# Kernel tuning notes

Hardware: AMD Instinct MI355X
Metric: run time of the kernel (lower is better)

The kernel has to match this reference:

```python
import jax, jax.numpy as jnp
import numpy as np

BLANK = 1
NEG = -1e30


def ctc_loss_mean(logprobs, targets, input_lengths, target_lengths):
    """CTC loss, log-space forward DP, matching torch.nn.CTCLoss(blank=1, reduction='mean').
    logprobs: [B,T,V] log-softmaxed; targets: [B,L] int; lengths: [B] int."""
    B, T, V = logprobs.shape
    L = targets.shape[1]
    S = 2 * L + 1  # extended label seq: blank interleaved
    ext = jnp.full((B, S), BLANK, dtype=targets.dtype)
    ext = ext.at[:, 1::2].set(targets)
    # lp_ext[b,t,s] = logprobs[b,t,ext[b,s]]
    lp_ext = jnp.take_along_axis(logprobs, jnp.broadcast_to(ext[:, None, :], (B, T, S)), axis=2)
    ext_m2 = jnp.pad(ext, ((0, 0), (2, 0)), constant_values=BLANK)[:, :S]
    skip_ok = (ext != BLANK) & (ext != ext_m2)  # [B,S] allow s-2 transition

    alpha = jnp.full((B, S), NEG, dtype=logprobs.dtype)
    alpha = alpha.at[:, 0].set(lp_ext[:, 0, 0])
    alpha = alpha.at[:, 1].set(jnp.where(target_lengths > 0, lp_ext[:, 0, 1], NEG))

    def step(alpha, inp):
        lp_t, t = inp  # lp_t: [B,S]
        a1 = jnp.pad(alpha, ((0, 0), (1, 0)), constant_values=NEG)[:, :S]
        a2 = jnp.pad(alpha, ((0, 0), (2, 0)), constant_values=NEG)[:, :S]
        a2 = jnp.where(skip_ok, a2, NEG)
        new = jnp.logaddexp(jnp.logaddexp(alpha, a1), a2) + lp_t
        alpha = jnp.where((t < input_lengths)[:, None], new, alpha)
        return alpha, None

    lp_tbs = jnp.transpose(lp_ext, (1, 0, 2))  # [T,B,S]
    alpha, _ = jax.lax.scan(step, alpha, (lp_tbs[1:], jnp.arange(1, T)))

    idx_last = 2 * target_lengths  # final blank position
    idx_prev = jnp.maximum(idx_last - 1, 0)
    a_last = jnp.take_along_axis(alpha, idx_last[:, None], axis=1)[:, 0]
    a_prev = jnp.where(target_lengths > 0,
                       jnp.take_along_axis(alpha, idx_prev[:, None], axis=1)[:, 0], NEG)
    per_sample = -jnp.logaddexp(a_last, a_prev)
    tl = jnp.maximum(target_lengths, 1).astype(logprobs.dtype)
    return jnp.mean(per_sample / tl)  # torch 'mean': divide by target_len, then batch mean


def setup_inputs() -> dict:
    key = jax.random.key(0)
    ks = jax.random.split(key, 8)
    B, Ssrc, D, STRIDE, V, L = 32, 512, 512, 4, 512, 256
    representation = jax.random.normal(ks[0], (B, Ssrc, D), dtype=jnp.float32)
    encoder_mask = jnp.ones((B, Ssrc), dtype=bool)
    targets = jax.random.randint(ks[1], (B, L), 2, V)  # avoid blank=1 and 0
    target_mask = jnp.ones((B, L), dtype=bool)
    def lin(k, fin, fout):
        return jax.random.normal(k, (fin, fout), dtype=jnp.float32) / np.sqrt(fin)
    return {
        "representation": representation,
        "encoder_mask": encoder_mask,
        "targets": targets,
        "target_mask": target_mask,
        "W_exp": lin(ks[2], D, STRIDE * D),
        "b_exp": jnp.zeros((STRIDE * D,), jnp.float32),
        "W1": lin(ks[3], D, 2 * D),
        "b1": jnp.zeros((2 * D,), jnp.float32),
        "W2": lin(ks[4], 2 * D, V),
        "b2": jnp.zeros((V,), jnp.float32),
    }


def reference(representation, encoder_mask, targets, target_mask,
              W_exp, b_exp, W1, b1, W2, b2):
    B = representation.shape[0]
    dim = W_exp.shape[0]
    seq_lengths = encoder_mask.astype(jnp.int32).sum(1)
    stride = W_exp.shape[1] // dim
    # expand: Linear(dim, stride*dim) then fold stride into time axis
    states = (jnp.einsum("bsd,de->bse", representation, W_exp) + b_exp).reshape(B, -1, dim)
    h = jax.nn.relu(jnp.einsum("btd,dh->bth", states, W1) + b1)
    logits = jnp.einsum("bth,hv->btv", h, W2) + b2  # dropout: eval-mode identity
    logprobs = jax.nn.log_softmax(logits, axis=-1)
    target_lengths = target_mask.astype(jnp.int32).sum(1)
    out_lengths = stride * seq_lengths
    loss = ctc_loss_mean(logprobs, targets, out_lengths, target_lengths)
    loss = jnp.where(jnp.isnan(loss) | jnp.isinf(loss), jnp.zeros_like(loss), loss)
    return logprobs, out_lengths, loss
```

## Files before the change

kernel.cpp:

```cpp
#include <hip/hip_runtime.h>
#include <math.h>

#define B_ 32
#define SSRC 512
#define D_ 512
#define STRIDE_ 4
#define V_ 512
#define L_ 256
#define T_ (SSRC * STRIDE_)
#define S_ (2 * L_ + 1)
#define BLANKI 1
#define PSTRIDE 264
#define BOOST 4096.0f
#define BOOST_BITS 12

typedef __attribute__((ext_vector_type(8))) short bf16x8;
typedef __attribute__((ext_vector_type(4))) float f32x4;

__device__ __forceinline__ unsigned short bf16r(float x) {
    unsigned u = __float_as_uint(x);
    return (unsigned short)((u + 0x7fffu + ((u >> 16) & 1u)) >> 16);
}
__device__ __forceinline__ float bf2f(unsigned short u) {
    return __uint_as_float((unsigned)u << 16);
}
__device__ __forceinline__ void gl_lds16(const unsigned short* g, unsigned short* l) {
    __builtin_amdgcn_global_load_lds(
        (const __attribute__((address_space(1))) unsigned int*)g,
        (__attribute__((address_space(3))) unsigned int*)l, 16, 0, 0);
}

__global__ __launch_bounds__(256) void combine_bias(
    const float* __restrict__ b_exp, const float* __restrict__ W1,
    const float* __restrict__ b1, float* __restrict__ bc)
{
    int j = blockIdx.x * 256 + threadIdx.x;
    int k = j >> 10, h = j & 1023;
    float s = b1[h];
    const float* be = b_exp + k * 512;
    for (int d = 0; d < 512; ++d)
        s = fmaf(be[d], W1[d * 1024 + h], s);
    bc[j] = s;
}

__global__ __launch_bounds__(256) void transpose_cvt(
    const float* __restrict__ in, unsigned short* __restrict__ out, int R, int C)
{
// ... 70 lines not shown
        for (int mi = 0; mi < 4; ++mi)
            af[mi] = *(const bf16x8*)&As[cur][wm + mi * 16 + (lane & 15)][(lane >> 4) * 8];
#pragma unroll
        for (int ni = 0; ni < 4; ++ni)
            bfr[ni] = *(const bf16x8*)&Bs[cur][wn + ni * 16 + (lane & 15)][(lane >> 4) * 8];
#pragma unroll
        for (int mi = 0; mi < 4; ++mi)
#pragma unroll
            for (int ni = 0; ni < 4; ++ni)
                acc[mi][ni] = __builtin_amdgcn_mfma_f32_16x16x32_bf16(
                    af[mi], bfr[ni], acc[mi][ni], 0, 0, 0);
    }

#pragma unroll
    for (int ni = 0; ni < 4; ++ni) {
        int gcol = bn + wn + ni * 16 + (lane & 15);
        float bv = BIAS ? bias[gcol] : 0.f;
#pragma unroll
        for (int mi = 0; mi < 4; ++mi) {
#pragma unroll
            for (int q2 = 0; q2 < 4; ++q2) {
                int grow = bm + wm + mi * 16 + ((lane >> 4) << 2) + q2;
                float x = acc[mi][ni][q2] + bv;
                if (RELU) x = fmaxf(x, 0.f);
                if (OUTBF16)
                    Cb[(size_t)grow * ldc + gcol] = bf16r(x);
                else
                    Cf[(size_t)grow * ldc + gcol] = x;
            }
        }
    }
}

__global__ __launch_bounds__(1024) void gemm2_lsm(
    const unsigned short* __restrict__ H,
    const unsigned short* __restrict__ W2T,
    const float* __restrict__ b2,
    const int* __restrict__ targets,
    float* __restrict__ lp,
    unsigned short* __restrict__ P)
{
    __shared__ __align__(16) char SMEM[81920];
    unsigned short* As = (unsigned short*)SMEM;
    unsigned short* Bs = (unsigned short*)(SMEM + 16384);
    float* redm = (float*)SMEM;
    float* reds = (float*)(SMEM + 4096);
    unsigned short* prt = (unsigned short*)(SMEM + 8192);
    int* s_tg = (int*)(SMEM + 8192 + 65536);

    const int tid = threadIdx.x;
    const int wid = tid >> 6, lane = tid & 63;
    const int wr = wid >> 3, wc = wid & 7;
    const int r0 = blockIdx.x * 128;
    const int b = r0 >> 11;

    auto stage = [&](int buf, int k0) {
#pragma unroll
        for (int ii = 0; ii < 3; ++ii) {
            int issue = wid + 16 * ii;
            if (issue < 8) {
                int rr = issue * 16;
                gl_lds16(H + (size_t)(r0 + rr + (lane >> 2)) * 1024 + k0 + (lane & 3) * 8,
                         &As[buf * 4096 + rr * 32]);
            } else if (issue < 40) {
                int rr = (issue - 8) * 16;
                gl_lds16(W2T + (size_t)(rr + (lane >> 2)) * 1024 + k0 + (lane & 3) * 8,
                         &Bs[buf * 16384 + rr * 32]);
            }
        }
    };

    f32x4 acc[4][4] = {};
    stage(0, 0);
    for (int t = 0; t < 32; ++t) {
        const int cur = t & 1;
        __syncthreads();
        if (t + 1 < 32) stage(cur ^ 1, (t + 1) * 32);
        bf16x8 af[4], bfr[4];
#pragma unroll
        for (int mi = 0; mi < 4; ++mi)
            af[mi] = *(const bf16x8*)&As[cur * 4096 +
                        (wr * 64 + mi * 16 + (lane & 15)) * 32 + (lane >> 4) * 8];
#pragma unroll
        for (int ni = 0; ni < 4; ++ni)
            bfr[ni] = *(const bf16x8*)&Bs[cur * 16384 +
                        (wc * 64 + ni * 16 + (lane & 15)) * 32 + (lane >> 4) * 8];
#pragma unroll
// ... 77 lines not shown
            for (int g = 1; g < 8; ++g) st += reds[g * 128 + row];
            rm[mi][q] = rm[mi][q] + logf(st);
        }

#pragma unroll
    for (int p = 0; p < 2; ++p) {
        if (wr == p) {
#pragma unroll
            for (int mi = 0; mi < 4; ++mi)
#pragma unroll
                for (int q = 0; q < 4; ++q) {
                    int rloc = mi * 16 + ((lane >> 4) << 2) + q;
                    int row = wr * 64 + rloc;
#pragma unroll
                    for (int ni = 0; ni < 4; ++ni) {
                        int col = wc * 64 + ni * 16 + (lane & 15);
                        float lpv = acc[mi][ni][q] - rm[mi][q];
                        lp[(size_t)(r0 + row) * 512 + col] = lpv;
                        prt[rloc * 512 + col] = bf16r(expf(lpv) * BOOST);
                    }
                }
        }
        __syncthreads();
        if (tid < 514) {
            int j = tid % 257;
            int rh = tid / 257;
            int col = (j < 256) ? s_tg[j] : BLANKI;
#pragma unroll 4
            for (int r = rh * 32; r < rh * 32 + 32; ++r)
                P[(size_t)(r0 + p * 64 + r) * PSTRIDE + j] = prt[r * 512 + col];
        }
        __syncthreads();
    }
}

struct Pr5 { float pb, p1, p3, p5, p7; };

__device__ __forceinline__ Pr5 ldrowf(const unsigned short* rp, int l)
{
    ushort4 q = *(const ushort4*)(rp + 4 * l);
    Pr5 r;
    r.pb = bf2f(rp[256]);
    r.p1 = bf2f(q.x); r.p3 = bf2f(q.y); r.p5 = bf2f(q.z); r.p7 = bf2f(q.w);
    return r;
}

#define REP16(OP) OP(0) OP(1) OP(2) OP(3) OP(4) OP(5) OP(6) OP(7) \
                  OP(8) OP(9) OP(10) OP(11) OP(12) OP(13) OP(14) OP(15)

__global__ __launch_bounds__(512) void ctc_fwd_bwd(
    const unsigned short* __restrict__ P,
    const int* __restrict__ enc_mask, const int* __restrict__ targets,
    const int* __restrict__ tgt_mask,
    float* __restrict__ out_len_f,
    double* __restrict__ AV, double* __restrict__ BV,
    int* __restrict__ EF, int* __restrict__ EB,
    int* __restrict__ ILv, int* __restrict__ tl_out)
{
    const int wid = threadIdx.x >> 6;
    const int l = threadIdx.x & 63;
    const int task = blockIdx.x * 8 + wid;
    const int b = task & 31;
    const bool isf = task < 32;

    int se = 0, st = 0;
    {
        const int* em = enc_mask + (size_t)b * SSRC;
#pragma unroll
        for (int i = 0; i < 8; ++i) se += (em[i * 64 + l] != 0) ? 1 : 0;
        const int* tm = tgt_mask + (size_t)b * L_;
#pragma unroll
        for (int i = 0; i < 4; ++i) st += (tm[i * 64 + l] != 0) ? 1 : 0;
#pragma unroll
        for (int off = 32; off; off >>= 1) {
            se += __shfl_xor(se, off);
            st += __shfl_xor(st, off);
        }
    }
    const int tl = st;
    const int IL = STRIDE_ * se;
    const int h = (IL > 0) ? ((IL - 1) >> 1) : 0;

    const int4 tg = ((const int4*)(targets + (size_t)b * L_))[l];
    int prevw = __shfl_up(tg.w, 1);
    if (l == 0) prevw = BLANKI;
    const bool k1 = (tg.x != BLANKI) && (tg.x != prevw);
    const bool k3 = (tg.y != BLANKI) && (tg.y != tg.x);
    const bool k5 = (tg.z != BLANKI) && (tg.z != tg.y);
    const bool k7 = (tg.w != BLANKI) && (tg.w != tg.z);

    const unsigned short* Pb = P + (size_t)b * T_ * PSTRIDE;

    double a0 = 0, a1 = 0, a2 = 0, a3 = 0, a4 = 0, a5 = 0, a6 = 0, a7 = 0, a8 = 0;
    int Ei = 0;

    auto rescale9 = [&]() {
        double m = fmax(fmax(fmax(a0, a1), fmax(a2, a3)),
                        fmax(fmax(a4, a5), fmax(fmax(a6, a7), a8)));
        int e = (int)((__double_as_longlong(m) >> 52) & 0x7ff);
#pragma unroll
        for (int off = 1; off < 64; off <<= 1) {
            int o = __shfl_xor(e, off);
            e = o > e ? o : e;
        }
        int sh = 1023 - e;
        double sc = __longlong_as_double(((long long)(sh + 1023)) << 52);
        Ei += e - 1023;
        a0 *= sc; a1 *= sc; a2 *= sc; a3 *= sc; a4 *= sc;
        a5 *= sc; a6 *= sc; a7 *= sc; a8 *= sc;
    };

    if (isf) {
        if (l == 0) {
            a0 = (double)bf2f(Pb[256]);
            if (tl > 0) a1 = (double)bf2f(Pb[0]);
        }
        auto fstep = [&](const Pr5& r) {
            double pb = (double)r.pb, p1 = (double)r.p1, p3 = (double)r.p3;
            double p5 = (double)r.p5, p7 = (double)r.p7;
            double u1 = __shfl_up(a7, 1);
            if (l == 0) u1 = 0.0;
            double n0 = (a0 + u1) * pb;
            double n1 = (a0 + a1 + (k1 ? u1 : 0.0)) * p1;
            double n2 = (a1 + a2) * pb;
            double n3 = (a2 + a3 + (k3 ? a1 : 0.0)) * p3;
            double n4 = (a3 + a4) * pb;
            double n5 = (a4 + a5 + (k5 ? a3 : 0.0)) * p5;
            double n6 = (a5 + a6) * pb;
            double n7 = (a6 + a7 + (k7 ? a5 : 0.0)) * p7;
            double n8 = (l == 63) ? (a7 + a8) * pb : 0.0;
            a0 = n0; a1 = n1; a2 = n2; a3 = n3; a4 = n4;
            a5 = n5; a6 = n6; a7 = n7; a8 = n8;
        };
        const int nst = h;
        if (nst > 0) {
            Pr5 q0, q1, q2, q3, q4, q5, q6, q7, q8, q9, q10, q11, q12, q13, q14, q15;
#define LDI(i) { int ti = 1 + i; if (ti > nst) ti = nst; \
                 q##i = ldrowf(Pb + (size_t)ti * PSTRIDE, l); }
            REP16(LDI)
#undef LDI
            int t = 1;
            while (t + 15 <= nst) {
#define STP(i) { fstep(q##i); int ti = t + 16 + i; if (ti > nst) ti = nst; \
                 q##i = ldrowf(Pb + (size_t)ti * PSTRIDE, l); }
                REP16(STP)
#undef STP
                rescale9();
                t += 16;
            }
            int rem = nst - t + 1;
#define TLS(i) if (i < rem) fstep(q##i);
            REP16(TLS)
#undef TLS
        }
        rescale9();
        double* av = AV + b * 520;
        av[l * 8 + 0] = a0; av[l * 8 + 1] = a1; av[l * 8 + 2] = a2; av[l * 8 + 3] = a3;
        av[l * 8 + 4] = a4; av[l * 8 + 5] = a5; av[l * 8 + 6] = a6; av[l * 8 + 7] = a7;
        if (l == 63) av[512] = a8;
        if (l == 0) {
            EF[b] = Ei; ILv[b] = IL; tl_out[b] = tl;
            out_len_f[b] = (float)IL;
        }
    } else {
        {
            int s0 = l * 8;
            int e0 = 2 * tl, e1 = 2 * tl - 1;
            a0 = (s0 + 0 == e0 || (tl > 0 && s0 + 0 == e1)) ? 1.0 : 0.0;
            a1 = (s0 + 1 == e0 || (tl > 0 && s0 + 1 == e1)) ? 1.0 : 0.0;
            a2 = (s0 + 2 == e0 || (tl > 0 && s0 + 2 == e1)) ? 1.0 : 0.0;
            a3 = (s0 + 3 == e0 || (tl > 0 && s0 + 3 == e1)) ? 1.0 : 0.0;
            a4 = (s0 + 4 == e0 || (tl > 0 && s0 + 4 == e1)) ? 1.0 : 0.0;
            a5 = (s0 + 5 == e0 || (tl > 0 && s0 + 5 == e1)) ? 1.0 : 0.0;
            a6 = (s0 + 6 == e0 || (tl > 0 && s0 + 6 == e1)) ? 1.0 : 0.0;
            a7 = (s0 + 7 == e0 || (tl > 0 && s0 + 7 == e1)) ? 1.0 : 0.0;
            if (l == 63) a8 = (512 == e0) ? 1.0 : 0.0;
        }
        float knff = __shfl_down(k1 ? 1.f : 0.f, 1);
        if (l == 63) knff = 0.f;
        const double knf = (double)knff;
        auto bstep = [&](const Pr5& r) {
            double pb = (double)r.pb, p1 = (double)r.p1, p3 = (double)r.p3;
            double p5 = (double)r.p5, p7 = (double)r.p7;
            double g0 = a0 * pb, g1 = a1 * p1, g2 = a2 * pb, g3 = a3 * p3;
            double g4 = a4 * pb, g5 = a5 * p5, g6 = a6 * pb, g7 = a7 * p7;
            double g8 = (l == 63) ? a8 * pb : 0.0;
            double d1 = __shfl_down(g0, 1);
            double d2 = __shfl_down(g1, 1);
            if (l == 63) { d1 = g8; d2 = 0.0; }
            double m0 = g0 + g1;
            double m1 = g1 + g2 + (k3 ? g3 : 0.0);
            double m2 = g2 + g3;
            double m3 = g3 + g4 + (k5 ? g5 : 0.0);
            double m4 = g4 + g5;
            double m5 = g5 + g6 + (k7 ? g7 : 0.0);
            double m6 = g6 + g7;
            double m7 = g7 + d1 + knf * d2;
            double m8 = (l == 63) ? g8 : 0.0;
            a0 = m0; a1 = m1; a2 = m2; a3 = m3; a4 = m4;
            a5 = m5; a6 = m6; a7 = m7; a8 = m8;
        };
        const int nbs = IL - 1 - h;
        if (nbs > 0) {
            const int rmin = h + 1;
            Pr5 q0, q1, q2, q3, q4, q5, q6, q7, q8, q9, q10, q11, q12, q13, q14, q15;
#define LDB(i) { int ri = IL - 1 - i; if (ri < rmin) ri = rmin; \
                 q##i = ldrowf(Pb + (size_t)ri * PSTRIDE, l); }
            REP16(LDB)
#undef LDB
            int j = 0;
            while (j + 16 <= nbs) {
#define STB(i) { bstep(q##i); int ri = IL - 1 - (j + 16 + i); if (ri < rmin) ri = rmin; \
                 q##i = ldrowf(Pb + (size_t)ri * PSTRIDE, l); }
                REP16(STB)
#undef STB
                rescale9();
                j += 16;
            }
            int rem = nbs - j;
#define TLB(i) if (i < rem) bstep(q##i);
            REP16(TLB)
#undef TLB
        }
        rescale9();
        double* bv = BV + b * 520;
        bv[l * 8 + 0] = a0; bv[l * 8 + 1] = a1; bv[l * 8 + 2] = a2; bv[l * 8 + 3] = a3;
        bv[l * 8 + 4] = a4; bv[l * 8 + 5] = a5; bv[l * 8 + 6] = a6; bv[l * 8 + 7] = a7;
        if (l == 63) bv[512] = a8;
        if (l == 0) EB[b] = Ei;
    }
}

__global__ __launch_bounds__(64) void ctc_combine(
    const double* __restrict__ AV, const double* __restrict__ BV,
    const int* __restrict__ EF, const int* __restrict__ EB,
    const int* __restrict__ ILv, float* __restrict__ per_sample)
{
    const int b = blockIdx.x, l = threadIdx.x;
    const double* av = AV + b * 520;
    const double* bv = BV + b * 520;
    double s = 0.0;
#pragma unroll
    for (int i = 0; i < 8; ++i)
        s += av[l * 8 + i] * bv[l * 8 + i];
    if (l == 63) s += av[512] * bv[512];
#pragma unroll
    for (int off = 1; off < 64; off <<= 1) s += __shfl_xor(s, off);
    if (l == 0) {
        double lg = log(s) +
            (double)(EF[b] + EB[b] - BOOST_BITS * ILv[b]) * 0.6931471805599453;
        per_sample[b] = -(float)lg;
    }
}

__global__ __launch_bounds__(64) void ctc_loss_final(
    const float* __restrict__ per_sample, const int* __restrict__ tl,
    float* __restrict__ out_loss)
{
    int tid = threadIdx.x;
    float v = 0.f;
    if (tid < B_) {
        int t = tl[tid] < 1 ? 1 : tl[tid];
        v = per_sample[tid] / (float)t;
// ... 10 lines not shown
extern "C" void kernel_launch(void* const* d_in, const int* in_sizes, int n_in,
                              void* d_out, int out_size, void* d_ws, size_t ws_size,
                              hipStream_t stream)
{
    (void)in_sizes; (void)n_in; (void)out_size; (void)ws_size;

    const float* rep      = (const float*)d_in[0];
    const int*   enc_mask = (const int*)d_in[1];
    const int*   targets  = (const int*)d_in[2];
    const int*   tgt_mask = (const int*)d_in[3];
    const float* W_exp    = (const float*)d_in[4];
    const float* b_exp    = (const float*)d_in[5];
    const float* W1       = (const float*)d_in[6];
    const float* b1       = (const float*)d_in[7];
    const float* W2       = (const float*)d_in[8];
    const float* b2       = (const float*)d_in[9];

    float* out       = (float*)d_out;
    float* logprobs  = out;
    float* out_len_f = out + (size_t)B_ * T_ * V_;
    float* out_loss  = out_len_f + B_;
    unsigned short* Hd = (unsigned short*)d_out;

    unsigned short* WcT = (unsigned short*)d_ws;
    float* bc           = (float*)(WcT + (size_t)4096 * 512);
    float* per_sample   = bc + 4096;
    int*   tl_out       = (int*)(per_sample + 64);
    unsigned short* P   = (unsigned short*)(tl_out + 64);
    double* AV          = (double*)(P + (size_t)65536 * PSTRIDE);
    double* BV          = AV + 32 * 520;
    int*   EF           = (int*)(BV + 32 * 520);
    int*   EB           = EF + 32;
    int*   ILv          = EB + 32;
    unsigned short* repb   = P;
    unsigned short* W_expb = P + (size_t)16384 * 512;
    unsigned short* W1T    = W_expb + (size_t)512 * 2048;
    unsigned short* W2T    = WcT;

    cvt_f32_bf16<<<8192, 256, 0, stream>>>(rep, repb, (16384 * 512) / 4);
    cvt_f32_bf16<<<1024, 256, 0, stream>>>(W_exp, W_expb, (512 * 2048) / 4);
    transpose_cvt<<<dim3(32, 16), dim3(32, 8), 0, stream>>>(W1, W1T, 512, 1024);

    gemm_mfma<false, true, false><<<dim3(4, 8, 4), 256, 0, stream>>>(
        W1T, 512, 0, W_expb, 2048, 512, WcT, 512, (long)1024 * 512, nullptr, 512);
    combine_bias<<<16, 256, 0, stream>>>(b_exp, W1, b1, bc);

    gemm_mfma<true, true, true><<<dim3(32, 128), 256, 0, stream>>>(
        repb, 512, 0, WcT, 512, 0, Hd, 4096, 0, bc, 512);

    transpose_cvt<<<dim3(16, 32), dim3(32, 8), 0, stream>>>(W2, W2T, 1024, 512);

    gemm2_lsm<<<512, 1024, 0, stream>>>(Hd, W2T, b2, targets, logprobs, P);

    ctc_fwd_bwd<<<8, 512, 0, stream>>>(P, enc_mask, targets, tgt_mask,
                                       out_len_f, AV, BV, EF, EB, ILv, tl_out);
    ctc_combine<<<32, 64, 0, stream>>>(AV, BV, EF, EB, ILv, per_sample);
    ctc_loss_final<<<1, 64, 0, stream>>>(per_sample, tl_out, out_loss);
}
```

Measured before the change: 488.1 us.

## Fuse CTC forward/backward into GEMM2 kernel with per-chunk readiness flags

Merges the CTC forward/backward recursion into the GEMM2+log-softmax kernel. The first 64 blocks act as single-wave consumers that spin on per-sample, per-128-row chunk flags. Producer blocks publish each chunk with a release atomic after a threadfence. Producer chunk order is interleaved from both ends, so the forward and backward consumers can start early. This overlaps the serial CTC recursion with the GEMM and removes one kernel launch. It relies on consumer blocks being scheduled alongside producers without deadlock, and each consumer block reserves a 1024-thread slot plus 80KB of LDS while only one wave does work.

```diff
diff --git a/kernel.cpp b/kernel.cpp
--- a/kernel.cpp
+++ b/kernel.cpp
@@ -13,6 +13,7 @@
 #define PSTRIDE 264
 #define BOOST 4096.0f
 #define BOOST_BITS 12
+#define NCONS 64
 
 typedef __attribute__((ext_vector_type(8))) short bf16x8;
 typedef __attribute__((ext_vector_type(4))) float f32x4;
@@ -149,15 +150,234 @@
     }
 }
 
-__global__ __launch_bounds__(1024) void gemm2_lsm(
+struct Pr5 { float pb, p1, p3, p5, p7; };
+
+__device__ __forceinline__ Pr5 ldrowf(const unsigned short* rp, int l)
+{
+    ushort4 q = *(const ushort4*)(rp + 4 * l);
+    Pr5 r;
+    r.pb = bf2f(rp[256]);
+    r.p1 = bf2f(q.x); r.p3 = bf2f(q.y); r.p5 = bf2f(q.z); r.p7 = bf2f(q.w);
+    return r;
+}
+
+#define REP16(OP) OP(0) OP(1) OP(2) OP(3) OP(4) OP(5) OP(6) OP(7) \
+                  OP(8) OP(9) OP(10) OP(11) OP(12) OP(13) OP(14) OP(15)
+
+__global__ __launch_bounds__(1024) void gemm2_lsm_ctc(
     const unsigned short* __restrict__ H,
     const unsigned short* __restrict__ W2T,
     const float* __restrict__ b2,
     const int* __restrict__ targets,
+    const int* __restrict__ enc_mask, const int* __restrict__ tgt_mask,
     float* __restrict__ lp,
-    unsigned short* __restrict__ P)
+    unsigned short* __restrict__ P,
+    int* __restrict__ flags,
+    float* __restrict__ out_len_f,
+    double* __restrict__ AV, double* __restrict__ BV,
+    int* __restrict__ EF, int* __restrict__ EB,
+    int* __restrict__ ILv, int* __restrict__ tl_out)
 {
     __shared__ __align__(16) char SMEM[81920];
+    const int tid = threadIdx.x;
+
+    if (blockIdx.x < NCONS) {
+        if (tid >= 64) return;
+        const int task = blockIdx.x;
+        const int b = task & 31;
+        const bool isf = task < 32;
+        const int l = tid;
+
+        int se = 0, st = 0;
+        {
+            const int* em = enc_mask + (size_t)b * SSRC;
+#pragma unroll
+            for (int i = 0; i < 8; ++i) se += (em[i * 64 + l] != 0) ? 1 : 0;
+            const int* tm = tgt_mask + (size_t)b * L_;
+#pragma unroll
+            for (int i = 0; i < 4; ++i) st += (tm[i * 64 + l] != 0) ? 1 : 0;
+#pragma unroll
+            for (int off = 32; off; off >>= 1) {
+                se += __shfl_xor(se, off);
+                st += __shfl_xor(st, off);
+            }
+        }
+        const int tl = st;
+        const int IL = STRIDE_ * se;
+        const int h = (IL > 0) ? ((IL - 1) >> 1) : 0;
+
+        const int4 tg = ((const int4*)(targets + (size_t)b * L_))[l];
+        int prevw = __shfl_up(tg.w, 1);
+        if (l == 0) prevw = BLANKI;
+        const bool k1 = (tg.x != BLANKI) && (tg.x != prevw);
+        const bool k3 = (tg.y != BLANKI) && (tg.y != tg.x);
+        const bool k5 = (tg.z != BLANKI) && (tg.z != tg.y);
+        const bool k7 = (tg.w != BLANKI) && (tg.w != tg.z);
+
+        const unsigned short* Pb = P + (size_t)b * T_ * PSTRIDE;
+
+        double a0 = 0, a1 = 0, a2 = 0, a3 = 0, a4 = 0, a5 = 0, a6 = 0, a7 = 0, a8 = 0;
+        int Ei = 0;
+
+        auto rescale9 = [&]() {
+            double m = fmax(fmax(fmax(a0, a1), fmax(a2, a3)),
+                            fmax(fmax(a4, a5), fmax(fmax(a6, a7), a8)));
+            int e = (int)((__double_as_longlong(m) >> 52) & 0x7ff);
+#pragma unroll
+            for (int off = 1; off < 64; off <<= 1) {
+                int o = __shfl_xor(e, off);
+                e = o > e ? o : e;
+            }
+            int sh = 1023 - e;
+            double sc = __longlong_as_double(((long long)(sh + 1023)) << 52);
+            Ei += e - 1023;
+            a0 *= sc; a1 *= sc; a2 *= sc; a3 *= sc; a4 *= sc;
+            a5 *= sc; a6 *= sc; a7 *= sc; a8 *= sc;
+        };
+        auto waitflag = [&](int c) {
+            const int f = b * 16 + c;
+            while (__hip_atomic_load(&flags[f], __ATOMIC_ACQUIRE,
+                                     __HIP_MEMORY_SCOPE_AGENT) == 0)
+                __builtin_amdgcn_s_sleep(16);
+        };
+
+        if (isf) {
+            int nw = 0;
+            auto waitup = [&](int row) {
+                int tc = row >> 7; if (tc > 15) tc = 15;
+                while (nw <= tc) { waitflag(nw); ++nw; }
+            };
+            waitup(0);
+            if (l == 0) {
+                a0 = (double)bf2f(Pb[256]);
+                if (tl > 0) a1 = (double)bf2f(Pb[0]);
+            }
+            auto fstep = [&](const Pr5& r) {
+                double pb = (double)r.pb, p1 = (double)r.p1, p3 = (double)r.p3;
+                double p5 = (double)r.p5, p7 = (double)r.p7;
+                double u1 = __shfl_up(a7, 1);
+                if (l == 0) u1 = 0.0;
+                double n0 = (a0 + u1) * pb;
+                double n1 = (a0 + a1 + (k1 ? u1 : 0.0)) * p1;
+                double n2 = (a1 + a2) * pb;
+                double n3 = (a2 + a3 + (k3 ? a1 : 0.0)) * p3;
+                double n4 = (a3 + a4) * pb;
+                double n5 = (a4 + a5 + (k5 ? a3 : 0.0)) * p5;
+                double n6 = (a5 + a6) * pb;
+                double n7 = (a6 + a7 + (k7 ? a5 : 0.0)) * p7;
+                double n8 = (l == 63) ? (a7 + a8) * pb : 0.0;
+                a0 = n0; a1 = n1; a2 = n2; a3 = n3; a4 = n4;
+                a5 = n5; a6 = n6; a7 = n7; a8 = n8;
+            };
+            const int nst = h;
+            if (nst > 0) {
+                waitup(nst < 47 ? nst : 47);
+                Pr5 q0, q1, q2, q3, q4, q5, q6, q7, q8, q9, q10, q11, q12, q13, q14, q15;
+#define LDI(i) { int ti = 1 + i; if (ti > nst) ti = nst; \
+                 q##i = ldrowf(Pb + (size_t)ti * PSTRIDE, l); }
+                REP16(LDI)
+#undef LDI
+                int t = 1;
+                while (t + 15 <= nst) {
+                    { int r2 = t + 47; if (r2 > nst) r2 = nst; waitup(r2); }
+#define STP(i) { fstep(q##i); int ti = t + 16 + i; if (ti > nst) ti = nst; \
+                 q##i = ldrowf(Pb + (size_t)ti * PSTRIDE, l); }
+                    REP16(STP)
+#undef STP
+                    rescale9();
+                    t += 16;
+                }
+                int rem = nst - t + 1;
+#define TLS(i) if (i < rem) fstep(q##i);
+                REP16(TLS)
+#undef TLS
+            }
+            rescale9();
+            double* av = AV + b * 520;
+            av[l * 8 + 0] = a0; av[l * 8 + 1] = a1; av[l * 8 + 2] = a2; av[l * 8 + 3] = a3;
+            av[l * 8 + 4] = a4; av[l * 8 + 5] = a5; av[l * 8 + 6] = a6; av[l * 8 + 7] = a7;
+            if (l == 63) av[512] = a8;
+            if (l == 0) {
+                EF[b] = Ei; ILv[b] = IL; tl_out[b] = tl;
+                out_len_f[b] = (float)IL;
+            }
+        } else {
+            int nb = 15;
+            auto waitdn = [&](int row) {
+                int tc = row >> 7; if (tc < 0) tc = 0;
+                while (nb >= tc) { waitflag(nb); --nb; }
+            };
+            {
+                int s0 = l * 8;
+                int e0 = 2 * tl, e1 = 2 * tl - 1;
+                a0 = (s0 + 0 == e0 || (tl > 0 && s0 + 0 == e1)) ? 1.0 : 0.0;
+                a1 = (s0 + 1 == e0 || (tl > 0 && s0 + 1 == e1)) ? 1.0 : 0.0;
+                a2 = (s0 + 2 == e0 || (tl > 0 && s0 + 2 == e1)) ? 1.0 : 0.0;
+                a3 = (s0 + 3 == e0 || (tl > 0 && s0 + 3 == e1)) ? 1.0 : 0.0;
+                a4 = (s0 + 4 == e0 || (tl > 0 && s0 + 4 == e1)) ? 1.0 : 0.0;
+                a5 = (s0 + 5 == e0 || (tl > 0 && s0 + 5 == e1)) ? 1.0 : 0.0;
+                a6 = (s0 + 6 == e0 || (tl > 0 && s0 + 6 == e1)) ? 1.0 : 0.0;
+                a7 = (s0 + 7 == e0 || (tl > 0 && s0 + 7 == e1)) ? 1.0 : 0.0;
+                if (l == 63) a8 = (512 == e0) ? 1.0 : 0.0;
+            }
+            float knff = __shfl_down(k1 ? 1.f : 0.f, 1);
+            if (l == 63) knff = 0.f;
+            const double knf = (double)knff;
+            auto bstep = [&](const Pr5& r) {
+                double pb = (double)r.pb, p1 = (double)r.p1, p3 = (double)r.p3;
+                double p5 = (double)r.p5, p7 = (double)r.p7;
+                double g0 = a0 * pb, g1 = a1 * p1, g2 = a2 * pb, g3 = a3 * p3;
+                double g4 = a4 * pb, g5 = a5 * p5, g6 = a6 * pb, g7 = a7 * p7;
+                double g8 = (l == 63) ? a8 * pb : 0.0;
+                double d1 = __shfl_down(g0, 1);
+                double d2 = __shfl_down(g1, 1);
+                if (l == 63) { d1 = g8; d2 = 0.0; }
+                double m0 = g0 + g1;
+                double m1 = g1 + g2 + (k3 ? g3 : 0.0);
+                double m2 = g2 + g3;
+                double m3 = g3 + g4 + (k5 ? g5 : 0.0);
+                double m4 = g4 + g5;
+                double m5 = g5 + g6 + (k7 ? g7 : 0.0);
+                double m6 = g6 + g7;
+                double m7 = g7 + d1 + knf * d2;
+                double m8 = (l == 63) ? g8 : 0.0;
+                a0 = m0; a1 = m1; a2 = m2; a3 = m3; a4 = m4;
+                a5 = m5; a6 = m6; a7 = m7; a8 = m8;
+            };
+            const int nbs = IL - 1 - h;
+            if (nbs > 0) {
+                const int rmin = h + 1;
+                { int r2 = IL - 1 - 47; if (r2 < rmin) r2 = rmin; waitdn(r2); }
+                Pr5 q0, q1, q2, q3, q4, q5, q6, q7, q8, q9, q10, q11, q12, q13, q14, q15;
+#define LDB(i) { int ri = IL - 1 - i; if (ri < rmin) ri = rmin; \
+                 q##i = ldrowf(Pb + (size_t)ri * PSTRIDE, l); }
+                REP16(LDB)
+#undef LDB
+                int j = 0;
+                while (j + 16 <= nbs) {
+                    { int r2 = IL - 1 - (j + 47); if (r2 < rmin) r2 = rmin; waitdn(r2); }
+#define STB(i) { bstep(q##i); int ri = IL - 1 - (j + 16 + i); if (ri < rmin) ri = rmin; \
+                 q##i = ldrowf(Pb + (size_t)ri * PSTRIDE, l); }
+                    REP16(STB)
+#undef STB
+                    rescale9();
+                    j += 16;
+                }
+                int rem = nbs - j;
+#define TLB(i) if (i < rem) bstep(q##i);
+                REP16(TLB)
+#undef TLB
+            }
+            rescale9();
+            double* bv = BV + b * 520;
+            bv[l * 8 + 0] = a0; bv[l * 8 + 1] = a1; bv[l * 8 + 2] = a2; bv[l * 8 + 3] = a3;
+            bv[l * 8 + 4] = a4; bv[l * 8 + 5] = a5; bv[l * 8 + 6] = a6; bv[l * 8 + 7] = a7;
+            if (l == 63) bv[512] = a8;
+            if (l == 0) EB[b] = Ei;
+        }
+        return;
+    }
+
     unsigned short* As = (unsigned short*)SMEM;
     unsigned short* Bs = (unsigned short*)(SMEM + 16384);
     float* redm = (float*)SMEM;
@@ -165,11 +385,15 @@
     unsigned short* prt = (unsigned short*)(SMEM + 8192);
     int* s_tg = (int*)(SMEM + 8192 + 65536);
 
-    const int tid = threadIdx.x;
+    const int pid = blockIdx.x - NCONS;
+    const int smp = pid & 31;
+    const int pc = pid >> 5;
+    const int chk = (pc & 1) ? (15 - (pc >> 1)) : (pc >> 1);
+    const int r0 = smp * 2048 + chk * 128;
+    const int b = smp;
+
     const int wid = tid >> 6, lane = tid & 63;
     const int wr = wid >> 3, wc = wid & 7;
-    const int r0 = blockIdx.x * 128;
-    const int b = r0 >> 11;
 
     auto stage = [&](int buf, int k0) {
 #pragma unroll
@@ -313,203 +537,11 @@
         }
         __syncthreads();
     }
-}
-
-struct Pr5 { float pb, p1, p3, p5, p7; };
-
-__device__ __forceinline__ Pr5 ldrowf(const unsigned short* rp, int l)
-{
-    ushort4 q = *(const ushort4*)(rp + 4 * l);
-    Pr5 r;
-    r.pb = bf2f(rp[256]);
-    r.p1 = bf2f(q.x); r.p3 = bf2f(q.y); r.p5 = bf2f(q.z); r.p7 = bf2f(q.w);
-    return r;
-}
-
-#define REP16(OP) OP(0) OP(1) OP(2) OP(3) OP(4) OP(5) OP(6) OP(7) \
-                  OP(8) OP(9) OP(10) OP(11) OP(12) OP(13) OP(14) OP(15)
-
-__global__ __launch_bounds__(512) void ctc_fwd_bwd(
-    const unsigned short* __restrict__ P,
-    const int* __restrict__ enc_mask, const int* __restrict__ targets,
-    const int* __restrict__ tgt_mask,
-    float* __restrict__ out_len_f,
-    double* __restrict__ AV, double* __restrict__ BV,
-    int* __restrict__ EF, int* __restrict__ EB,
-    int* __restrict__ ILv, int* __restrict__ tl_out)
-{
-    const int wid = threadIdx.x >> 6;
-    const int l = threadIdx.x & 63;
-    const int task = blockIdx.x * 8 + wid;
-    const int b = task & 31;
-    const bool isf = task < 32;
-
-    int se = 0, st = 0;
-    {
-        const int* em = enc_mask + (size_t)b * SSRC;
-#pragma unroll
-        for (int i = 0; i < 8; ++i) se += (em[i * 64 + l] != 0) ? 1 : 0;
-        const int* tm = tgt_mask + (size_t)b * L_;
-#pragma unroll
-        for (int i = 0; i < 4; ++i) st += (tm[i * 64 + l] != 0) ? 1 : 0;
-#pragma unroll
-        for (int off = 32; off; off >>= 1) {
-            se += __shfl_xor(se, off);
-            st += __shfl_xor(st, off);
-        }
-    }
-    const int tl = st;
-    const int IL = STRIDE_ * se;
-    const int h = (IL > 0) ? ((IL - 1) >> 1) : 0;
-
-    const int4 tg = ((const int4*)(targets + (size_t)b * L_))[l];
-    int prevw = __shfl_up(tg.w, 1);
-    if (l == 0) prevw = BLANKI;
-    const bool k1 = (tg.x != BLANKI) && (tg.x != prevw);
-    const bool k3 = (tg.y != BLANKI) && (tg.y != tg.x);
-    const bool k5 = (tg.z != BLANKI) && (tg.z != tg.y);
-    const bool k7 = (tg.w != BLANKI) && (tg.w != tg.z);
-
-    const unsigned short* Pb = P + (size_t)b * T_ * PSTRIDE;
-
-    double a0 = 0, a1 = 0, a2 = 0, a3 = 0, a4 = 0, a5 = 0, a6 = 0, a7 = 0, a8 = 0;
-    int Ei = 0;
-
-    auto rescale9 = [&]() {
-        double m = fmax(fmax(fmax(a0, a1), fmax(a2, a3)),
-                        fmax(fmax(a4, a5), fmax(fmax(a6, a7), a8)));
-        int e = (int)((__double_as_longlong(m) >> 52) & 0x7ff);
-#pragma unroll
-        for (int off = 1; off < 64; off <<= 1) {
-            int o = __shfl_xor(e, off);
-            e = o > e ? o : e;
-        }
-        int sh = 1023 - e;
-        double sc = __longlong_as_double(((long long)(sh + 1023)) << 52);
-        Ei += e - 1023;
-        a0 *= sc; a1 *= sc; a2 *= sc; a3 *= sc; a4 *= sc;
-        a5 *= sc; a6 *= sc; a7 *= sc; a8 *= sc;
-    };
-
-    if (isf) {
-        if (l == 0) {
-            a0 = (double)bf2f(Pb[256]);
-            if (tl > 0) a1 = (double)bf2f(Pb[0]);
-        }
-        auto fstep = [&](const Pr5& r) {
-            double pb = (double)r.pb, p1 = (double)r.p1, p3 = (double)r.p3;
-            double p5 = (double)r.p5, p7 = (double)r.p7;
-            double u1 = __shfl_up(a7, 1);
-            if (l == 0) u1 = 0.0;
-            double n0 = (a0 + u1) * pb;
-            double n1 = (a0 + a1 + (k1 ? u1 : 0.0)) * p1;
-            double n2 = (a1 + a2) * pb;
-            double n3 = (a2 + a3 + (k3 ? a1 : 0.0)) * p3;
-            double n4 = (a3 + a4) * pb;
-            double n5 = (a4 + a5 + (k5 ? a3 : 0.0)) * p5;
-            double n6 = (a5 + a6) * pb;
-            double n7 = (a6 + a7 + (k7 ? a5 : 0.0)) * p7;
-            double n8 = (l == 63) ? (a7 + a8) * pb : 0.0;
-            a0 = n0; a1 = n1; a2 = n2; a3 = n3; a4 = n4;
-            a5 = n5; a6 = n6; a7 = n7; a8 = n8;
-        };
-        const int nst = h;
-        if (nst > 0) {
-            Pr5 q0, q1, q2, q3, q4, q5, q6, q7, q8, q9, q10, q11, q12, q13, q14, q15;
-#define LDI(i) { int ti = 1 + i; if (ti > nst) ti = nst; \
-                 q##i = ldrowf(Pb + (size_t)ti * PSTRIDE, l); }
-            REP16(LDI)
-#undef LDI
-            int t = 1;
-            while (t + 15 <= nst) {
-#define STP(i) { fstep(q##i); int ti = t + 16 + i; if (ti > nst) ti = nst; \
-                 q##i = ldrowf(Pb + (size_t)ti * PSTRIDE, l); }
-                REP16(STP)
-#undef STP
-                rescale9();
-                t += 16;
-            }
-            int rem = nst - t + 1;
-#define TLS(i) if (i < rem) fstep(q##i);
-            REP16(TLS)
-#undef TLS
-        }
-        rescale9();
-        double* av = AV + b * 520;
-        av[l * 8 + 0] = a0; av[l * 8 + 1] = a1; av[l * 8 + 2] = a2; av[l * 8 + 3] = a3;
-        av[l * 8 + 4] = a4; av[l * 8 + 5] = a5; av[l * 8 + 6] = a6; av[l * 8 + 7] = a7;
-        if (l == 63) av[512] = a8;
-        if (l == 0) {
-            EF[b] = Ei; ILv[b] = IL; tl_out[b] = tl;
-            out_len_f[b] = (float)IL;
-        }
-    } else {
-        {
-            int s0 = l * 8;
-            int e0 = 2 * tl, e1 = 2 * tl - 1;
-            a0 = (s0 + 0 == e0 || (tl > 0 && s0 + 0 == e1)) ? 1.0 : 0.0;
-            a1 = (s0 + 1 == e0 || (tl > 0 && s0 + 1 == e1)) ? 1.0 : 0.0;
-            a2 = (s0 + 2 == e0 || (tl > 0 && s0 + 2 == e1)) ? 1.0 : 0.0;
-            a3 = (s0 + 3 == e0 || (tl > 0 && s0 + 3 == e1)) ? 1.0 : 0.0;
-            a4 = (s0 + 4 == e0 || (tl > 0 && s0 + 4 == e1)) ? 1.0 : 0.0;
-            a5 = (s0 + 5 == e0 || (tl > 0 && s0 + 5 == e1)) ? 1.0 : 0.0;
-            a6 = (s0 + 6 == e0 || (tl > 0 && s0 + 6 == e1)) ? 1.0 : 0.0;
-            a7 = (s0 + 7 == e0 || (tl > 0 && s0 + 7 == e1)) ? 1.0 : 0.0;
-            if (l == 63) a8 = (512 == e0) ? 1.0 : 0.0;
-        }
-        float knff = __shfl_down(k1 ? 1.f : 0.f, 1);
-        if (l == 63) knff = 0.f;
-        const double knf = (double)knff;
-        auto bstep = [&](const Pr5& r) {
-            double pb = (double)r.pb, p1 = (double)r.p1, p3 = (double)r.p3;
-            double p5 = (double)r.p5, p7 = (double)r.p7;
-            double g0 = a0 * pb, g1 = a1 * p1, g2 = a2 * pb, g3 = a3 * p3;
-            double g4 = a4 * pb, g5 = a5 * p5, g6 = a6 * pb, g7 = a7 * p7;
-            double g8 = (l == 63) ? a8 * pb : 0.0;
-            double d1 = __shfl_down(g0, 1);
-            double d2 = __shfl_down(g1, 1);
-            if (l == 63) { d1 = g8; d2 = 0.0; }
-            double m0 = g0 + g1;
-            double m1 = g1 + g2 + (k3 ? g3 : 0.0);
-            double m2 = g2 + g3;
-            double m3 = g3 + g4 + (k5 ? g5 : 0.0);
-            double m4 = g4 + g5;
-            double m5 = g5 + g6 + (k7 ? g7 : 0.0);
-            double m6 = g6 + g7;
-            double m7 = g7 + d1 + knf * d2;
-            double m8 = (l == 63) ? g8 : 0.0;
-            a0 = m0; a1 = m1; a2 = m2; a3 = m3; a4 = m4;
-            a5 = m5; a6 = m6; a7 = m7; a8 = m8;
-        };
-        const int nbs = IL - 1 - h;
-        if (nbs > 0) {
-            const int rmin = h + 1;
-            Pr5 q0, q1, q2, q3, q4, q5, q6, q7, q8, q9, q10, q11, q12, q13, q14, q15;
-#define LDB(i) { int ri = IL - 1 - i; if (ri < rmin) ri = rmin; \
-                 q##i = ldrowf(Pb + (size_t)ri * PSTRIDE, l); }
-            REP16(LDB)
-#undef LDB
-            int j = 0;
-            while (j + 16 <= nbs) {
-#define STB(i) { bstep(q##i); int ri = IL - 1 - (j + 16 + i); if (ri < rmin) ri = rmin; \
-                 q##i = ldrowf(Pb + (size_t)ri * PSTRIDE, l); }
-                REP16(STB)
-#undef STB
-                rescale9();
-                j += 16;
-            }
-            int rem = nbs - j;
-#define TLB(i) if (i < rem) bstep(q##i);
-            REP16(TLB)
-#undef TLB
-        }
-        rescale9();
-        double* bv = BV + b * 520;
-        bv[l * 8 + 0] = a0; bv[l * 8 + 1] = a1; bv[l * 8 + 2] = a2; bv[l * 8 + 3] = a3;
-        bv[l * 8 + 4] = a4; bv[l * 8 + 5] = a5; bv[l * 8 + 6] = a6; bv[l * 8 + 7] = a7;
-        if (l == 63) bv[512] = a8;
-        if (l == 0) EB[b] = Ei;
-    }
+
+    __threadfence();
+    if (tid == 0)
+        __hip_atomic_store(&flags[smp * 16 + chk], 1, __ATOMIC_RELEASE,
+                           __HIP_MEMORY_SCOPE_AGENT);
 }
 
 __global__ __launch_bounds__(64) void ctc_combine(
@@ -586,6 +618,7 @@
     int*   EF           = (int*)(BV + 32 * 520);
     int*   EB           = EF + 32;
     int*   ILv          = EB + 32;
+    int*   flags        = ILv + 32;
     unsigned short* repb   = P;
     unsigned short* W_expb = P + (size_t)16384 * 512;
     unsigned short* W1T    = W_expb + (size_t)512 * 2048;
@@ -604,10 +637,11 @@
 
     transpose_cvt<<<dim3(16, 32), dim3(32, 8), 0, stream>>>(W2, W2T, 1024, 512);
 
-    gemm2_lsm<<<512, 1024, 0, stream>>>(Hd, W2T, b2, targets, logprobs, P);
-
-    ctc_fwd_bwd<<<8, 512, 0, stream>>>(P, enc_mask, targets, tgt_mask,
-                                       out_len_f, AV, BV, EF, EB, ILv, tl_out);
+    hipMemsetAsync(flags, 0, 512 * sizeof(int), stream);
+    gemm2_lsm_ctc<<<NCONS + 512, 1024, 0, stream>>>(
+        Hd, W2T, b2, targets, enc_mask, tgt_mask, logprobs, P, flags,
+        out_len_f, AV, BV, EF, EB, ILv, tl_out);
+
     ctc_combine<<<32, 64, 0, stream>>>(AV, BV, EF, EB, ILv, per_sample);
     ctc_loss_final<<<1, 64, 0, stream>>>(per_sample, tl_out, out_loss);
 }
```

After: 872.6 us. +78.8%, slower.

## Interleave CTC forward and backward recursions in one wavefront per sample

Applied to the files above, without the earlier changes.

Merges the separate forward and backward wavefronts (64 wavefronts in 8 blocks) into one 64-thread wavefront per batch sample that steps the alpha and beta recursions in alternation. The two independent dependency chains give the instruction scheduler ILP to hide shuffle and FP64 latency inside a single wave. The prefetch depth per direction drops from 16 rows to 8 to bound register use, and the kernel now runs 32 single-wave blocks. Rescaling happens every 8 steps instead of 16.

```diff
diff --git a/kernel.cpp b/kernel.cpp
--- a/kernel.cpp
+++ b/kernel.cpp
@@ -326,10 +326,9 @@
     return r;
 }
 
-#define REP16(OP) OP(0) OP(1) OP(2) OP(3) OP(4) OP(5) OP(6) OP(7) \
-                  OP(8) OP(9) OP(10) OP(11) OP(12) OP(13) OP(14) OP(15)
-
-__global__ __launch_bounds__(512) void ctc_fwd_bwd(
+#define REP8(OP) OP(0) OP(1) OP(2) OP(3) OP(4) OP(5) OP(6) OP(7)
+
+__global__ __launch_bounds__(64) void ctc_fb2(
     const unsigned short* __restrict__ P,
     const int* __restrict__ enc_mask, const int* __restrict__ targets,
     const int* __restrict__ tgt_mask,
@@ -338,11 +337,8 @@
     int* __restrict__ EF, int* __restrict__ EB,
     int* __restrict__ ILv, int* __restrict__ tl_out)
 {
-    const int wid = threadIdx.x >> 6;
-    const int l = threadIdx.x & 63;
-    const int task = blockIdx.x * 8 + wid;
-    const int b = task & 31;
-    const bool isf = task < 32;
+    const int b = blockIdx.x;
+    const int l = threadIdx.x;
 
     int se = 0, st = 0;
     {
@@ -369,146 +365,155 @@
     const bool k3 = (tg.y != BLANKI) && (tg.y != tg.x);
     const bool k5 = (tg.z != BLANKI) && (tg.z != tg.y);
     const bool k7 = (tg.w != BLANKI) && (tg.w != tg.z);
+    float knff = __shfl_down(k1 ? 1.f : 0.f, 1);
+    if (l == 63) knff = 0.f;
+    const double knf = (double)knff;
 
     const unsigned short* Pb = P + (size_t)b * T_ * PSTRIDE;
 
-    double a0 = 0, a1 = 0, a2 = 0, a3 = 0, a4 = 0, a5 = 0, a6 = 0, a7 = 0, a8 = 0;
-    int Ei = 0;
-
-    auto rescale9 = [&]() {
-        double m = fmax(fmax(fmax(a0, a1), fmax(a2, a3)),
-                        fmax(fmax(a4, a5), fmax(fmax(a6, a7), a8)));
+    double f0 = 0, f1 = 0, f2 = 0, f3 = 0, f4 = 0, f5 = 0, f6 = 0, f7 = 0, f8 = 0;
+    int EiF = 0;
+    double g0a = 0, g1a = 0, g2a = 0, g3a = 0, g4a = 0, g5a = 0, g6a = 0, g7a = 0, g8a = 0;
+    int EiB = 0;
+
+    if (l == 0) {
+        f0 = (double)bf2f(Pb[256]);
+        if (tl > 0) f1 = (double)bf2f(Pb[0]);
+    }
+    {
+        int s0 = l * 8;
+        int e0 = 2 * tl, e1 = 2 * tl - 1;
+        g0a = (s0 + 0 == e0 || (tl > 0 && s0 + 0 == e1)) ? 1.0 : 0.0;
+        g1a = (s0 + 1 == e0 || (tl > 0 && s0 + 1 == e1)) ? 1.0 : 0.0;
+        g2a = (s0 + 2 == e0 || (tl > 0 && s0 + 2 == e1)) ? 1.0 : 0.0;
+        g3a = (s0 + 3 == e0 || (tl > 0 && s0 + 3 == e1)) ? 1.0 : 0.0;
+        g4a = (s0 + 4 == e0 || (tl > 0 && s0 + 4 == e1)) ? 1.0 : 0.0;
+        g5a = (s0 + 5 == e0 || (tl > 0 && s0 + 5 == e1)) ? 1.0 : 0.0;
+        g6a = (s0 + 6 == e0 || (tl > 0 && s0 + 6 == e1)) ? 1.0 : 0.0;
+        g7a = (s0 + 7 == e0 || (tl > 0 && s0 + 7 == e1)) ? 1.0 : 0.0;
+        if (l == 63) g8a = (512 == e0) ? 1.0 : 0.0;
+    }
+
+    auto fstep = [&](const Pr5& r) {
+        double pb = (double)r.pb, p1 = (double)r.p1, p3 = (double)r.p3;
+        double p5 = (double)r.p5, p7 = (double)r.p7;
+        double u1 = __shfl_up(f7, 1);
+        if (l == 0) u1 = 0.0;
+        double n0 = (f0 + u1) * pb;
+        double n1 = (f0 + f1 + (k1 ? u1 : 0.0)) * p1;
+        double n2 = (f1 + f2) * pb;
+        double n3 = (f2 + f3 + (k3 ? f1 : 0.0)) * p3;
+        double n4 = (f3 + f4) * pb;
+        double n5 = (f4 + f5 + (k5 ? f3 : 0.0)) * p5;
+        double n6 = (f5 + f6) * pb;
+        double n7 = (f6 + f7 + (k7 ? f5 : 0.0)) * p7;
+        double n8 = (l == 63) ? (f7 + f8) * pb : 0.0;
+        f0 = n0; f1 = n1; f2 = n2; f3 = n3; f4 = n4;
+        f5 = n5; f6 = n6; f7 = n7; f8 = n8;
+    };
+    auto bstep = [&](const Pr5& r) {
+        double pb = (double)r.pb, p1 = (double)r.p1, p3 = (double)r.p3;
+        double p5 = (double)r.p5, p7 = (double)r.p7;
+        double g0 = g0a * pb, g1 = g1a * p1, g2 = g2a * pb, g3 = g3a * p3;
+        double g4 = g4a * pb, g5 = g5a * p5, g6 = g6a * pb, g7 = g7a * p7;
+        double g8 = (l == 63) ? g8a * pb : 0.0;
+        double d1 = __shfl_down(g0, 1);
+        double d2 = __shfl_down(g1, 1);
+        if (l == 63) { d1 = g8; d2 = 0.0; }
+        double m0 = g0 + g1;
+        double m1 = g1 + g2 + (k3 ? g3 : 0.0);
+        double m2 = g2 + g3;
+        double m3 = g3 + g4 + (k5 ? g5 : 0.0);
+        double m4 = g4 + g5;
+        double m5 = g5 + g6 + (k7 ? g7 : 0.0);
+        double m6 = g6 + g7;
+        double m7 = g7 + d1 + knf * d2;
+        double m8 = (l == 63) ? g8 : 0.0;
+        g0a = m0; g1a = m1; g2a = m2; g3a = m3; g4a = m4;
+        g5a = m5; g6a = m6; g7a = m7; g8a = m8;
+    };
+    auto rescaleF = [&]() {
+        double m = fmax(fmax(fmax(f0, f1), fmax(f2, f3)),
+                        fmax(fmax(f4, f5), fmax(fmax(f6, f7), f8)));
         int e = (int)((__double_as_longlong(m) >> 52) & 0x7ff);
 #pragma unroll
         for (int off = 1; off < 64; off <<= 1) {
             int o = __shfl_xor(e, off);
             e = o > e ? o : e;
         }
-        int sh = 1023 - e;
-        double sc = __longlong_as_double(((long long)(sh + 1023)) << 52);
-        Ei += e - 1023;
-        a0 *= sc; a1 *= sc; a2 *= sc; a3 *= sc; a4 *= sc;
-        a5 *= sc; a6 *= sc; a7 *= sc; a8 *= sc;
+        double sc = __longlong_as_double(((long long)(2046 - e)) << 52);
+        EiF += e - 1023;
+        f0 *= sc; f1 *= sc; f2 *= sc; f3 *= sc; f4 *= sc;
+        f5 *= sc; f6 *= sc; f7 *= sc; f8 *= sc;
     };
-
-    if (isf) {
-        if (l == 0) {
-            a0 = (double)bf2f(Pb[256]);
-            if (tl > 0) a1 = (double)bf2f(Pb[0]);
-        }
-        auto fstep = [&](const Pr5& r) {
-            double pb = (double)r.pb, p1 = (double)r.p1, p3 = (double)r.p3;
-            double p5 = (double)r.p5, p7 = (double)r.p7;
-            double u1 = __shfl_up(a7, 1);
-            if (l == 0) u1 = 0.0;
-            double n0 = (a0 + u1) * pb;
-            double n1 = (a0 + a1 + (k1 ? u1 : 0.0)) * p1;
-            double n2 = (a1 + a2) * pb;
-            double n3 = (a2 + a3 + (k3 ? a1 : 0.0)) * p3;
-            double n4 = (a3 + a4) * pb;
-            double n5 = (a4 + a5 + (k5 ? a3 : 0.0)) * p5;
-            double n6 = (a5 + a6) * pb;
-            double n7 = (a6 + a7 + (k7 ? a5 : 0.0)) * p7;
-            double n8 = (l == 63) ? (a7 + a8) * pb : 0.0;
-            a0 = n0; a1 = n1; a2 = n2; a3 = n3; a4 = n4;
-            a5 = n5; a6 = n6; a7 = n7; a8 = n8;
-        };
-        const int nst = h;
-        if (nst > 0) {
-            Pr5 q0, q1, q2, q3, q4, q5, q6, q7, q8, q9, q10, q11, q12, q13, q14, q15;
-#define LDI(i) { int ti = 1 + i; if (ti > nst) ti = nst; \
-                 q##i = ldrowf(Pb + (size_t)ti * PSTRIDE, l); }
-            REP16(LDI)
-#undef LDI
-            int t = 1;
-            while (t + 15 <= nst) {
-#define STP(i) { fstep(q##i); int ti = t + 16 + i; if (ti > nst) ti = nst; \
-                 q##i = ldrowf(Pb + (size_t)ti * PSTRIDE, l); }
-                REP16(STP)
-#undef STP
-                rescale9();
-                t += 16;
-            }
-            int rem = nst - t + 1;
-#define TLS(i) if (i < rem) fstep(q##i);
-            REP16(TLS)
-#undef TLS
-        }
-        rescale9();
-        double* av = AV + b * 520;
-        av[l * 8 + 0] = a0; av[l * 8 + 1] = a1; av[l * 8 + 2] = a2; av[l * 8 + 3] = a3;
-        av[l * 8 + 4] = a4; av[l * 8 + 5] = a5; av[l * 8 + 6] = a6; av[l * 8 + 7] = a7;
-        if (l == 63) av[512] = a8;
-        if (l == 0) {
-            EF[b] = Ei; ILv[b] = IL; tl_out[b] = tl;
-            out_len_f[b] = (float)IL;
-        }
-    } else {
-        {
-            int s0 = l * 8;
-            int e0 = 2 * tl, e1 = 2 * tl - 1;
-            a0 = (s0 + 0 == e0 || (tl > 0 && s0 + 0 == e1)) ? 1.0 : 0.0;
-            a1 = (s0 + 1 == e0 || (tl > 0 && s0 + 1 == e1)) ? 1.0 : 0.0;
-            a2 = (s0 + 2 == e0 || (tl > 0 && s0 + 2 == e1)) ? 1.0 : 0.0;
-            a3 = (s0 + 3 == e0 || (tl > 0 && s0 + 3 == e1)) ? 1.0 : 0.0;
-            a4 = (s0 + 4 == e0 || (tl > 0 && s0 + 4 == e1)) ? 1.0 : 0.0;
-            a5 = (s0 + 5 == e0 || (tl > 0 && s0 + 5 == e1)) ? 1.0 : 0.0;
-            a6 = (s0 + 6 == e0 || (tl > 0 && s0 + 6 == e1)) ? 1.0 : 0.0;
-            a7 = (s0 + 7 == e0 || (tl > 0 && s0 + 7 == e1)) ? 1.0 : 0.0;
-            if (l == 63) a8 = (512 == e0) ? 1.0 : 0.0;
-        }
-        float knff = __shfl_down(k1 ? 1.f : 0.f, 1);
-        if (l == 63) knff = 0.f;
-        const double knf = (double)knff;
-        auto bstep = [&](const Pr5& r) {
-            double pb = (double)r.pb, p1 = (double)r.p1, p3 = (double)r.p3;
-            double p5 = (double)r.p5, p7 = (double)r.p7;
-            double g0 = a0 * pb, g1 = a1 * p1, g2 = a2 * pb, g3 = a3 * p3;
-            double g4 = a4 * pb, g5 = a5 * p5, g6 = a6 * pb, g7 = a7 * p7;
-            double g8 = (l == 63) ? a8 * pb : 0.0;
-            double d1 = __shfl_down(g0, 1);
-            double d2 = __shfl_down(g1, 1);
-            if (l == 63) { d1 = g8; d2 = 0.0; }
-            double m0 = g0 + g1;
-            double m1 = g1 + g2 + (k3 ? g3 : 0.0);
-            double m2 = g2 + g3;
-            double m3 = g3 + g4 + (k5 ? g5 : 0.0);
-            double m4 = g4 + g5;
-            double m5 = g5 + g6 + (k7 ? g7 : 0.0);
-            double m6 = g6 + g7;
-            double m7 = g7 + d1 + knf * d2;
-            double m8 = (l == 63) ? g8 : 0.0;
-            a0 = m0; a1 = m1; a2 = m2; a3 = m3; a4 = m4;
-            a5 = m5; a6 = m6; a7 = m7; a8 = m8;
-        };
-        const int nbs = IL - 1 - h;
-        if (nbs > 0) {
-            const int rmin = h + 1;
-            Pr5 q0, q1, q2, q3, q4, q5, q6, q7, q8, q9, q10, q11, q12, q13, q14, q15;
-#define LDB(i) { int ri = IL - 1 - i; if (ri < rmin) ri = rmin; \
-                 q##i = ldrowf(Pb + (size_t)ri * PSTRIDE, l); }
-            REP16(LDB)
-#undef LDB
-            int j = 0;
-            while (j + 16 <= nbs) {
-#define STB(i) { bstep(q##i); int ri = IL - 1 - (j + 16 + i); if (ri < rmin) ri = rmin; \
-                 q##i = ldrowf(Pb + (size_t)ri * PSTRIDE, l); }
-                REP16(STB)
-#undef STB
-                rescale9();
-                j += 16;
-            }
-            int rem = nbs - j;
-#define TLB(i) if (i < rem) bstep(q##i);
-            REP16(TLB)
+    auto rescaleB = [&]() {
+        double m = fmax(fmax(fmax(g0a, g1a), fmax(g2a, g3a)),
+                        fmax(fmax(g4a, g5a), fmax(fmax(g6a, g7a), g8a)));
+        int e = (int)((__double_as_longlong(m) >> 52) & 0x7ff);
+#pragma unroll
+        for (int off = 1; off < 64; off <<= 1) {
+            int o = __shfl_xor(e, off);
+            e = o > e ? o : e;
+        }
+        double sc = __longlong_as_double(((long long)(2046 - e)) << 52);
+        EiB += e - 1023;
+        g0a *= sc; g1a *= sc; g2a *= sc; g3a *= sc; g4a *= sc;
+        g5a *= sc; g6a *= sc; g7a *= sc; g8a *= sc;
+    };
+
+    const int nf = h;
+    const int nb = IL - 1 - h;
+    const int rmin = h + 1;
+
+    if (nf > 0 || nb > 0) {
+        Pr5 qf0, qf1, qf2, qf3, qf4, qf5, qf6, qf7;
+        Pr5 qb0, qb1, qb2, qb3, qb4, qb5, qb6, qb7;
+#define LDF(i) { int ti = 1 + i; if (ti > nf) ti = nf > 0 ? nf : 1; \
+                 qf##i = ldrowf(Pb + (size_t)ti * PSTRIDE, l); }
+#define LDBW(i) { int ri = IL - 1 - i; if (ri < rmin) ri = rmin; if (ri < 0) ri = 0; \
+                 qb##i = ldrowf(Pb + (size_t)ri * PSTRIDE, l); }
+        REP8(LDF)
+        REP8(LDBW)
+#undef LDF
+#undef LDBW
+        int t = 1, j = 0;
+        while (t + 7 <= nf && j + 7 <= nb) {
+#define PSTEP(i) { \
+            fstep(qf##i); \
+            { int ti = t + 8 + i; if (ti > nf) ti = nf; \
+              qf##i = ldrowf(Pb + (size_t)ti * PSTRIDE, l); } \
+            bstep(qb##i); \
+            { int ri = IL - 1 - (j + 8 + i); if (ri < rmin) ri = rmin; \
+              qb##i = ldrowf(Pb + (size_t)ri * PSTRIDE, l); } }
+            REP8(PSTEP)
+#undef PSTEP
+            rescaleF();
+            rescaleB();
+            t += 8; j += 8;
+        }
+        int remf = nf - t + 1; if (remf < 0) remf = 0;
+        int remb = nb - j;     if (remb < 0) remb = 0;
+#define TLF(i) if (i < remf) fstep(qf##i);
+        REP8(TLF)
+#undef TLF
+#define TLB(i) if (i < remb) bstep(qb##i);
+        REP8(TLB)
 #undef TLB
-        }
-        rescale9();
-        double* bv = BV + b * 520;
-        bv[l * 8 + 0] = a0; bv[l * 8 + 1] = a1; bv[l * 8 + 2] = a2; bv[l * 8 + 3] = a3;
-        bv[l * 8 + 4] = a4; bv[l * 8 + 5] = a5; bv[l * 8 + 6] = a6; bv[l * 8 + 7] = a7;
-        if (l == 63) bv[512] = a8;
-        if (l == 0) EB[b] = Ei;
+    }
+    rescaleF();
+    rescaleB();
+
+    double* av = AV + b * 520;
+    av[l * 8 + 0] = f0; av[l * 8 + 1] = f1; av[l * 8 + 2] = f2; av[l * 8 + 3] = f3;
+    av[l * 8 + 4] = f4; av[l * 8 + 5] = f5; av[l * 8 + 6] = f6; av[l * 8 + 7] = f7;
+    if (l == 63) av[512] = f8;
+    double* bv = BV + b * 520;
+    bv[l * 8 + 0] = g0a; bv[l * 8 + 1] = g1a; bv[l * 8 + 2] = g2a; bv[l * 8 + 3] = g3a;
+    bv[l * 8 + 4] = g4a; bv[l * 8 + 5] = g5a; bv[l * 8 + 6] = g6a; bv[l * 8 + 7] = g7a;
+    if (l == 63) bv[512] = g8a;
+    if (l == 0) {
+        EF[b] = EiF; EB[b] = EiB; ILv[b] = IL; tl_out[b] = tl;
+        out_len_f[b] = (float)IL;
     }
 }
 
@@ -606,8 +611,8 @@
 
     gemm2_lsm<<<512, 1024, 0, stream>>>(Hd, W2T, b2, targets, logprobs, P);
 
-    ctc_fwd_bwd<<<8, 512, 0, stream>>>(P, enc_mask, targets, tgt_mask,
-                                       out_len_f, AV, BV, EF, EB, ILv, tl_out);
+    ctc_fb2<<<B_, 64, 0, stream>>>(P, enc_mask, targets, tgt_mask,
+                                   out_len_f, AV, BV, EF, EB, ILv, tl_out);
     ctc_combine<<<32, 64, 0, stream>>>(AV, BV, EF, EB, ILv, per_sample);
     ctc_loss_final<<<1, 64, 0, stream>>>(per_sample, tl_out, out_loss);
 }
```

New measurement: 550.1 us. 1.13x slower.
